# Performance work log

Measured on AMD Instinct MI355X. Metric: run time of the kernel, lower is better.

The kernel has to match this reference:

```python
import jax, jax.numpy as jnp
import numpy as np

N = 50000
E = 400000
IN_DIM = 16
EMB = 32
HID = 128
HEADS = 4
LAYERS = 3
EPS_BN = 1e-5
NEG_SLOPE = 0.2


def setup_inputs() -> dict:
    key = jax.random.key(0)
    ks = jax.random.split(key, 16)
    s = 0.1
    C = HID  # per-head out channels (concat=False)
    inp = {
        "x": jax.random.normal(ks[0], (N, IN_DIM), jnp.float32),
        "edge_index": jax.random.randint(ks[1], (2, E), 0, N, jnp.int64),
        "emb": s * jax.random.normal(ks[2], (N, EMB), jnp.float32),
        "Wf": s * jax.random.normal(ks[3], (EMB, IN_DIM), jnp.float32),
        "bf": jnp.zeros((EMB,), jnp.float32),
        "Wc": s * jax.random.normal(ks[4], (HID, 2 * EMB), jnp.float32),
        "bc": jnp.zeros((HID,), jnp.float32),
        "Wl": s * jax.random.normal(ks[5], (LAYERS, HEADS * C, HID), jnp.float32),
        "a_src": s * jax.random.normal(ks[6], (LAYERS, HEADS, C), jnp.float32),
        "a_dst": s * jax.random.normal(ks[7], (LAYERS, HEADS, C), jnp.float32),
        "bl": jnp.zeros((LAYERS, C), jnp.float32),
        "gamma": jnp.ones((LAYERS, C), jnp.float32),
        "beta": jnp.zeros((LAYERS, C), jnp.float32),
        "Wout": s * jax.random.normal(ks[8], (1, HID), jnp.float32),
        "bout": jnp.zeros((1,), jnp.float32),
    }
    return inp


def _gat_layer(h, src, dst, W, a_s, a_d, b):
    n = h.shape[0]
    C = W.shape[0] // HEADS
    hp = (h @ W.T).reshape(n, HEADS, C)                # (N,H,C)
    al_s = jnp.sum(hp * a_s, axis=-1)                  # (N,H)
    al_d = jnp.sum(hp * a_d, axis=-1)                  # (N,H)
    e = jax.nn.leaky_relu(al_s[src] + al_d[dst], NEG_SLOPE)  # (E,H)
    m = jax.ops.segment_max(e, dst, num_segments=n)    # per-target max
    ex = jnp.exp(e - m[dst])
    denom = jax.ops.segment_sum(ex, dst, num_segments=n) + 1e-16
    alpha = ex / denom[dst]                            # (E,H)
    msg = hp[src] * alpha[..., None]                   # (E,H,C)
    out = jax.ops.segment_sum(msg, dst, num_segments=n)
    return jnp.mean(out, axis=1) + b                   # concat=False: head mean


def _bn(x, g, b):
    mu = jnp.mean(x, axis=0)
    var = jnp.var(x, axis=0)  # biased, as torch BN uses for normalization
    return (x - mu) * jax.lax.rsqrt(var + EPS_BN) * g + b


def reference(x, edge_index, emb, Wf, bf, Wc, bc, Wl, a_src, a_dst, bl, gamma, beta, Wout, bout):
    n = x.shape[0]
    loop = jnp.arange(n, dtype=edge_index.dtype)
    src = jnp.concatenate([edge_index[0], loop])       # add self loops
    dst = jnp.concatenate([edge_index[1], loop])
    feat = x @ Wf.T + bf
    h = jax.nn.relu(jnp.concatenate([emb, feat], axis=1) @ Wc.T + bc)
    prev_h = h
    for i in range(LAYERS):
        h = _gat_layer(h, src, dst, Wl[i], a_src[i], a_dst[i], bl[i])
        h = jax.nn.relu(_bn(h, gamma[i], beta[i]))
        if prev_h.shape == h.shape:
            h = h + prev_h
        prev_h = h
    out = h @ Wout.T + bout
    return jnp.clip(out, -10.0, 10.0)
```

## Files before the change

### kernel.cpp

```cpp
#include <hip/hip_runtime.h>
#include <hip/hip_bf16.h>
#include <math.h>

#define INDIM 16
#define EMBD 32
#define UDIM 64
#define HIDD 128
#define HEADS 4
#define LAYERS 3
#define MPAD 50048

typedef short v8s __attribute__((ext_vector_type(8)));
typedef float v4f __attribute__((ext_vector_type(4)));

__device__ __forceinline__ float lrelu(float x) { return x > 0.f ? x : 0.2f * x; }
__device__ __forceinline__ float bf2f(unsigned int bits16) {
    unsigned int u = bits16 << 16;
    return __builtin_bit_cast(float, u);
}
__device__ __forceinline__ unsigned short f2bf(float f) {
    unsigned int u = __builtin_bit_cast(unsigned int, f);
    unsigned int lsb = (u >> 16) & 1;
    u += 0x7fff + lsb;
    return (unsigned short)(u >> 16);
}

__global__ __launch_bounds__(256) void k_enc(const float* __restrict__ x,
                                             const float* __restrict__ emb,
                                             const float* __restrict__ Wf,
                                             const float* __restrict__ bf,
                                             unsigned short* __restrict__ u, int n) {
    int i = blockIdx.x * 256 + threadIdx.x;
    if (i >= n * EMBD) return;
    int node = i >> 5, j = i & 31;
    const float* xr = x + (size_t)node * INDIM;
    const float* wr = Wf + (size_t)j * INDIM;
    float s = bf[j];
#pragma unroll
    for (int k = 0; k < INDIM; k++) s += xr[k] * wr[k];
    u[(size_t)node * UDIM + EMBD + j] = f2bf(s);
    u[(size_t)node * UDIM + j] = f2bf(emb[(size_t)node * EMBD + j]);
}

__global__ __launch_bounds__(256) void k_prep_v(const float* __restrict__ Wl,
                                                unsigned short* __restrict__ Vb) {
    int i = blockIdx.x * 256 + threadIdx.x;
    if (i >= LAYERS * HIDD * 512) return;
    int l = i >> 16;
    int rem = i & 65535;
    int c = rem >> 9;
    int f = rem & 511;
    int h = f >> 7, k = f & 127;
    Vb[i] = f2bf(Wl[(size_t)l * 512 * HIDD + (size_t)(h * HIDD + c) * HIDD + k]);
}

__global__ __launch_bounds__(256) void k_prep_a(const float* __restrict__ Wl,
                                                const float* __restrict__ a_s,
                                                const float* __restrict__ a_d,
                                                float* __restrict__ ws, float* __restrict__ wd) {
    int i = blockIdx.x * 256 + threadIdx.x;
    if (i >= LAYERS * HEADS * HIDD) return;
    int l = i >> 9, h = (i >> 7) & 3, k = i & 127;
    const float* W = Wl + (size_t)l * 512 * HIDD;
    const float* as = a_s + l * 512 + h * HIDD;
    const float* ad = a_d + l * 512 + h * HIDD;
    float ss = 0.f, sd = 0.f;
    for (int c = 0; c < HIDD; c++) {
        float w = W[(size_t)(h * HIDD + c) * HIDD + k];
        ss += as[c] * w;
        sd += ad[c] * w;
    }
    ws[i] = ss;
    wd[i] = sd;
}

__global__ __launch_bounds__(256) void k_prep_wc(const float* __restrict__ Wc,
                                                 unsigned short* __restrict__ Wcb) {
    int i = blockIdx.x * 256 + threadIdx.x;
    if (i < HIDD * UDIM) Wcb[i] = f2bf(Wc[i]);
}

__global__ __launch_bounds__(256) void k_gemm_enc(const unsigned short* __restrict__ A,
                                                  const unsigned short* __restrict__ B,
                                                  const float* __restrict__ bias,
                                                  float* __restrict__ O,
                                                  unsigned short* __restrict__ Ob, int M) {
    const int K = UDIM;
    int tid = threadIdx.x;
    int lane = tid & 63, wid = tid >> 6;
    int wm = wid >> 1, wn = wid & 1;
    int bm = blockIdx.x * 128;
    int lr = lane & 15, lk = lane >> 4;
    v4f acc[4][4] = {};
    const unsigned short* Abase = A + (size_t)(bm + wm * 64 + lr) * K + lk * 8;
    const unsigned short* Bbase = B + (size_t)(wn * 64 + lr) * K + lk * 8;
#pragma unroll
    for (int kk = 0; kk < K / 32; kk++) {
        v8s a[4], b[4];
#pragma unroll
        for (int f = 0; f < 4; f++) {
            a[f] = *(const v8s*)(Abase + (size_t)(f * 16) * K + kk * 32);
            b[f] = *(const v8s*)(Bbase + (size_t)(f * 16) * K + kk * 32);
        }
#pragma unroll
        for (int i = 0; i < 4; i++)
#pragma unroll
            for (int j = 0; j < 4; j++)
                acc[i][j] = __builtin_amdgcn_mfma_f32_16x16x32_bf16(a[i], b[j], acc[i][j], 0, 0, 0);
    }
#pragma unroll
    for (int i = 0; i < 4; i++) {
#pragma unroll
        for (int r = 0; r < 4; r++) {
            int row = bm + wm * 64 + i * 16 + lk * 4 + r;
            if (row >= M) continue;
#pragma unroll
            for (int j = 0; j < 4; j++) {
                int col = wn * 64 + j * 16 + lr;
                float v = fmaxf(acc[i][j][r] + bias[col], 0.f);
                O[(size_t)row * HIDD + col] = v;
                Ob[(size_t)row * HIDD + col] = f2bf(v);
            }
        }
    }
}

__global__ __launch_bounds__(256) void k_deg(const int* __restrict__ ei, int* __restrict__ deg,
                                             int E, int tot) {
    int e = blockIdx.x * 256 + threadIdx.x;
    if (e >= tot) return;
    int dst = (e < E) ? ei[E + e] : (e - E);
    atomicAdd(&deg[dst], 1);
}

__global__ __launch_bounds__(256) void k_scan1(const int* __restrict__ deg,
                                               int* __restrict__ rowptr,
                                               int* __restrict__ partials, int n) {
    int tid = threadIdx.x;
    int i = blockIdx.x * 256 + tid;
    int v = (i < n) ? deg[i] : 0;
    __shared__ int sm[256];
    sm[tid] = v;
    __syncthreads();
    for (int off = 1; off < 256; off <<= 1) {
        int t = (tid >= off) ? sm[tid - off] : 0;
        __syncthreads();
        sm[tid] += t;
        __syncthreads();
    }
    if (i < n) rowptr[i] = sm[tid] - v;
    if (tid == 255) partials[blockIdx.x] = sm[255];
}

__global__ __launch_bounds__(256) void k_scan2(int* __restrict__ partials, int nb) {
    int tid = threadIdx.x;
    int v = (tid < nb) ? partials[tid] : 0;
    __shared__ int sm[256];
    sm[tid] = v;
    __syncthreads();
    for (int off = 1; off < 256; off <<= 1) {
        int t = (tid >= off) ? sm[tid - off] : 0;
        __syncthreads();
        sm[tid] += t;
        __syncthreads();
    }
    if (tid < nb) partials[tid] = sm[tid] - v;
}

__global__ __launch_bounds__(256) void k_scan3(const int* __restrict__ deg,
                                               const int* __restrict__ partials,
                                               int* __restrict__ rowptr,
                                               int* __restrict__ cursor, int n) {
    int i = blockIdx.x * 256 + threadIdx.x;
    if (i >= n) return;
    int r = rowptr[i] + partials[blockIdx.x];
    rowptr[i] = r;
    cursor[i] = r;
    if (i == n - 1) rowptr[n] = r + deg[i];
}

__global__ __launch_bounds__(256) void k_scatter(const int* __restrict__ ei, int* __restrict__ cursor,
                                                 int* __restrict__ csr_src, int E, int tot) {
    int e = blockIdx.x * 256 + threadIdx.x;
    if (e >= tot) return;
    int src = (e < E) ? ei[e] : (e - E);
    int dst = (e < E) ? ei[E + e] : (e - E);
    int pos = atomicAdd(&cursor[dst], 1);
    csr_src[pos] = src;
}

__global__ __launch_bounds__(256) void k_al0(const float* __restrict__ h,
                                             const float* __restrict__ ws,
                                             const float* __restrict__ wd,
                                             float* __restrict__ al_s, float* __restrict__ al_d,
                                             int n) {
    int wid = threadIdx.x >> 6, lane = threadIdx.x & 63;
    int node = blockIdx.x * 4 + wid;
    if (node >= n) return;
    float2 v = *(const float2*)(h + (size_t)node * HIDD + 2 * lane);
    float s[8];
#pragma unroll
    for (int hh = 0; hh < 4; hh++) {
        float2 w1 = *(const float2*)(ws + hh * HIDD + 2 * lane);
        float2 w2 = *(const float2*)(wd + hh * HIDD + 2 * lane);
        s[hh] = v.x * w1.x + v.y * w1.y;
        s[4 + hh] = v.x * w2.x + v.y * w2.y;
    }
#pragma unroll
    for (int o = 32; o; o >>= 1)
#pragma unroll
        for (int q = 0; q < 8; q++) s[q] += __shfl_xor(s[q], o);
    if (lane == 0) {
        *(float4*)(al_s + (size_t)node * 4) = make_float4(s[0], s[1], s[2], s[3]);
        *(float4*)(al_d + (size_t)node * 4) = make_float4(s[4], s[5], s[6], s[7]);
    }
}

__global__ __launch_bounds__(256) void k_layer(const int* __restrict__ rowptr,
                                               const int* __restrict__ csr_src,
                                               const float* __restrict__ al_s,
                                               const float* __restrict__ al_d,
                                               const unsigned short* __restrict__ hb,
                                               const unsigned short* __restrict__ Vb,
                                               float* __restrict__ agg,
                                               float* __restrict__ bns, int n) {
    __shared__ unsigned short G[16][520];
    __shared__ float s1[128], s2[128];
    int tid = threadIdx.x, lane = tid & 63, wid = tid >> 6;
    if (tid < 128) { s1[tid] = 0.f; s2[tid] = 0.f; }
    int node0 = blockIdx.x * 16;
    const float4* als4 = (const float4*)al_s;
    const unsigned int* h2 = (const unsigned int*)hb;
    unsigned int* Gw = (unsigned int*)G;

    for (int i = 0; i < 4; i++) {
        int lrow = wid * 4 + i;
        int node = node0 + lrow;
        float acc[4][2] = {};
        if (node < n) {
            int start = rowptr[node], end = rowptr[node + 1];
            int deg = end - start;
            float4 ad = ((const float4*)al_d)[node];
            if (deg <= 64) {
                bool act = lane < deg;
                int src_l = act ? csr_src[start + lane] : 0;
                float e0 = -3.0e38f, e1 = -3.0e38f, e2 = -3.0e38f, e3 = -3.0e38f;
                if (act) {
                    float4 as = als4[src_l];
                    e0 = lrelu(as.x + ad.x);
                    e1 = lrelu(as.y + ad.y);
                    e2 = lrelu(as.z + ad.z);
                    e3 = lrelu(as.w + ad.w);
                }
                float m0 = e0, m1 = e1, m2 = e2, m3 = e3;
#pragma unroll
                for (int o = 32; o; o >>= 1) {
                    m0 = fmaxf(m0, __shfl_xor(m0, o));
                    m1 = fmaxf(m1, __shfl_xor(m1, o));
                    m2 = fmaxf(m2, __shfl_xor(m2, o));
                    m3 = fmaxf(m3, __shfl_xor(m3, o));
                }
                float p0 = act ? expf(e0 - m0) : 0.f;
                float p1 = act ? expf(e1 - m1) : 0.f;
                float p2 = act ? expf(e2 - m2) : 0.f;
                float p3 = act ? expf(e3 - m3) : 0.f;
                float t0 = p0, t1 = p1, t2 = p2, t3 = p3;
#pragma unroll
                for (int o = 32; o; o >>= 1) {
                    t0 += __shfl_xor(t0, o);
                    t1 += __shfl_xor(t1, o);
                    t2 += __shfl_xor(t2, o);
                    t3 += __shfl_xor(t3, o);
                }
                float a0 = p0 / (t0 + 1e-16f), a1 = p1 / (t1 + 1e-16f);
                float a2 = p2 / (t2 + 1e-16f), a3 = p3 / (t3 + 1e-16f);
                int jj = 0;
                for (; jj + 2 <= deg; jj += 2) {
                    int sj0 = __shfl(src_l, jj), sj1 = __shfl(src_l, jj + 1);
                    unsigned int u0 = h2[(size_t)sj0 * 64 + lane];
                    unsigned int u1 = h2[(size_t)sj1 * 64 + lane];
                    float b00 = __shfl(a0, jj), b01 = __shfl(a1, jj);
                    float b02 = __shfl(a2, jj), b03 = __shfl(a3, jj);
                    float b10 = __shfl(a0, jj + 1), b11 = __shfl(a1, jj + 1);
                    float b12 = __shfl(a2, jj + 1), b13 = __shfl(a3, jj + 1);
                    float x00 = bf2f(u0 & 0xffff), x01 = bf2f(u0 >> 16);
                    float x10 = bf2f(u1 & 0xffff), x11 = bf2f(u1 >> 16);
                    acc[0][0] += b00 * x00 + b10 * x10; acc[0][1] += b00 * x01 + b10 * x11;
                    acc[1][0] += b01 * x00 + b11 * x10; acc[1][1] += b01 * x01 + b11 * x11;
                    acc[2][0] += b02 * x00 + b12 * x10; acc[2][1] += b02 * x01 + b12 * x11;
                    acc[3][0] += b03 * x00 + b13 * x10; acc[3][1] += b03 * x01 + b13 * x11;
                }
                if (jj < deg) {
                    int sj = __shfl(src_l, jj);
                    unsigned int uu = h2[(size_t)sj * 64 + lane];
                    float b0 = __shfl(a0, jj), b1 = __shfl(a1, jj);
                    float b2 = __shfl(a2, jj), b3 = __shfl(a3, jj);
                    float x0 = bf2f(uu & 0xffff), x1 = bf2f(uu >> 16);
                    acc[0][0] += b0 * x0; acc[0][1] += b0 * x1;
                    acc[1][0] += b1 * x0; acc[1][1] += b1 * x1;
                    acc[2][0] += b2 * x0; acc[2][1] += b2 * x1;
                    acc[3][0] += b3 * x0; acc[3][1] += b3 * x1;
                }
            } else {
                float m0 = -3.0e38f, m1 = -3.0e38f, m2 = -3.0e38f, m3 = -3.0e38f;
                for (int j = start + lane; j < end; j += 64) {
                    float4 as = als4[csr_src[j]];
                    m0 = fmaxf(m0, lrelu(as.x + ad.x));
                    m1 = fmaxf(m1, lrelu(as.y + ad.y));
                    m2 = fmaxf(m2, lrelu(as.z + ad.z));
                    m3 = fmaxf(m3, lrelu(as.w + ad.w));
                }
#pragma unroll
                for (int o = 32; o; o >>= 1) {
                    m0 = fmaxf(m0, __shfl_xor(m0, o));
                    m1 = fmaxf(m1, __shfl_xor(m1, o));
                    m2 = fmaxf(m2, __shfl_xor(m2, o));
                    m3 = fmaxf(m3, __shfl_xor(m3, o));
                }
                float t0 = 0.f, t1 = 0.f, t2 = 0.f, t3 = 0.f;
                for (int j = start + lane; j < end; j += 64) {
                    float4 as = als4[csr_src[j]];
                    t0 += expf(lrelu(as.x + ad.x) - m0);
                    t1 += expf(lrelu(as.y + ad.y) - m1);
                    t2 += expf(lrelu(as.z + ad.z) - m2);
                    t3 += expf(lrelu(as.w + ad.w) - m3);
                }
#pragma unroll
                for (int o = 32; o; o >>= 1) {
                    t0 += __shfl_xor(t0, o);
                    t1 += __shfl_xor(t1, o);
                    t2 += __shfl_xor(t2, o);
                    t3 += __shfl_xor(t3, o);
                }
                float i0 = 1.f / (t0 + 1e-16f), i1 = 1.f / (t1 + 1e-16f);
                float i2 = 1.f / (t2 + 1e-16f), i3 = 1.f / (t3 + 1e-16f);
                for (int base = start; base < end; base += 64) {
                    int cnt = min(64, end - base);
                    bool act = lane < cnt;
                    int src_l = act ? csr_src[base + lane] : 0;
                    float a0 = 0.f, a1 = 0.f, a2 = 0.f, a3 = 0.f;
                    if (act) {
                        float4 as = als4[src_l];
                        a0 = expf(lrelu(as.x + ad.x) - m0) * i0;
                        a1 = expf(lrelu(as.y + ad.y) - m1) * i1;
                        a2 = expf(lrelu(as.z + ad.z) - m2) * i2;
                        a3 = expf(lrelu(as.w + ad.w) - m3) * i3;
                    }
                    for (int jj = 0; jj < cnt; jj++) {
                        int sj = __shfl(src_l, jj);
                        float b0 = __shfl(a0, jj), b1 = __shfl(a1, jj);
                        float b2 = __shfl(a2, jj), b3 = __shfl(a3, jj);
                        unsigned int uu = h2[(size_t)sj * 64 + lane];
                        float x0 = bf2f(uu & 0xffff), x1 = bf2f(uu >> 16);
                        acc[0][0] += b0 * x0; acc[0][1] += b0 * x1;
                        acc[1][0] += b1 * x0; acc[1][1] += b1 * x1;
                        acc[2][0] += b2 * x0; acc[2][1] += b2 * x1;
                        acc[3][0] += b3 * x0; acc[3][1] += b3 * x1;
                    }
                }
            }
        }
#pragma unroll
        for (int hh = 0; hh < 4; hh++) {
            unsigned int p = (unsigned int)f2bf(acc[hh][0]) | ((unsigned int)f2bf(acc[hh][1]) << 16);
            Gw[lrow * 260 + hh * 64 + lane] = p;
        }
    }
    __syncthreads();

    int lr = lane & 15, lk = lane >> 4;
    v4f acc2[2] = {};
#pragma unroll
    for (int kk = 0; kk < 16; kk++) {
        v8s a = *(const v8s*)((const char*)G + lr * 1040 + kk * 64 + lk * 16);
        v8s b0 = *(const v8s*)(Vb + (size_t)(wid * 32 + lr) * 512 + kk * 32 + lk * 8);
        v8s b1 = *(const v8s*)(Vb + (size_t)(wid * 32 + 16 + lr) * 512 + kk * 32 + lk * 8);
        acc2[0] = __builtin_amdgcn_mfma_f32_16x16x32_bf16(a, b0, acc2[0], 0, 0, 0);
        acc2[1] = __builtin_amdgcn_mfma_f32_16x16x32_bf16(a, b1, acc2[1], 0, 0, 0);
    }
#pragma unroll
    for (int j = 0; j < 2; j++) {
        int col = wid * 32 + j * 16 + lr;
        float ls = 0.f, lq = 0.f;
#pragma unroll
        for (int r = 0; r < 4; r++) {
            int node = node0 + lk * 4 + r;
            float v = acc2[j][r];
            if (node < n) {
                agg[(size_t)node * HIDD + col] = v;
                ls += v;
                lq += v * v;
            }
        }
        atomicAdd(&s1[col], ls);
        atomicAdd(&s2[col], lq);
    }
    __syncthreads();
    if (tid < 128) {
        atomicAdd(&bns[tid], s1[tid]);
        atomicAdd(&bns[128 + tid], s2[tid]);
    }
}

template <int MODE>
__global__ __launch_bounds__(256) void k_apply(const float* __restrict__ agg,
                                               const float* __restrict__ bns,
                                               const float* __restrict__ gamma,
                                               const float* __restrict__ beta,
                                               float* __restrict__ h,
                                               unsigned short* __restrict__ hb,
                                               const float* __restrict__ ws,
                                               const float* __restrict__ wd,
                                               float* __restrict__ al_s,
                                               float* __restrict__ al_d,
                                               const float* __restrict__ Wout,
                                               const float* __restrict__ bout,
                                               float* __restrict__ out,
                                               float invn, int n) {
    int wid = threadIdx.x >> 6, lane = threadIdx.x & 63;
    int node = blockIdx.x * 4 + wid;
    if (node >= n) return;
    int c0 = 2 * lane, c1 = 2 * lane + 1;
    float2 ag = *(const float2*)(agg + (size_t)node * HIDD + c0);
    float2 ho = *(const float2*)(h + (size_t)node * HIDD + c0);
    float mu0 = bns[c0] * invn, mu1 = bns[c1] * invn;
    float va0 = bns[128 + c0] * invn - mu0 * mu0;
    float va1 = bns[128 + c1] * invn - mu1 * mu1;
    float sc0 = gamma[c0] * rsqrtf(0.0625f * va0 + 1e-5f);
    float sc1 = gamma[c1] * rsqrtf(0.0625f * va1 + 1e-5f);
    float v0 = fmaxf((ag.x - mu0) * 0.25f * sc0 + beta[c0], 0.f) + ho.x;
    float v1 = fmaxf((ag.y - mu1) * 0.25f * sc1 + beta[c1], 0.f) + ho.y;
    if (MODE == 0) {
        *(float2*)(h + (size_t)node * HIDD + c0) = make_float2(v0, v1);
        ((unsigned int*)hb)[(size_t)node * 64 + lane] =
            (unsigned int)f2bf(v0) | ((unsigned int)f2bf(v1) << 16);
        float s[8];
#pragma unroll
        for (int hh = 0; hh < 4; hh++) {
            float2 w1 = *(const float2*)(ws + hh * HIDD + c0);
            float2 w2 = *(const float2*)(wd + hh * HIDD + c0);
            s[hh] = v0 * w1.x + v1 * w1.y;
            s[4 + hh] = v0 * w2.x + v1 * w2.y;
        }
#pragma unroll
        for (int o = 32; o; o >>= 1)
#pragma unroll
            for (int q = 0; q < 8; q++) s[q] += __shfl_xor(s[q], o);
        if (lane == 0) {
            *(float4*)(al_s + (size_t)node * 4) = make_float4(s[0], s[1], s[2], s[3]);
            *(float4*)(al_d + (size_t)node * 4) = make_float4(s[4], s[5], s[6], s[7]);
        }
    } else {
        float2 w = *(const float2*)(Wout + c0);
        float p = v0 * w.x + v1 * w.y;
#pragma unroll
        for (int o = 32; o; o >>= 1) p += __shfl_xor(p, o);
        if (lane == 0) {
            float v = p + bout[0];
            out[node] = fminf(fmaxf(v, -10.f), 10.f);
        }
    }
}

extern "C" void kernel_launch(void* const* d_in, const int* in_sizes, int n_in,
                              void* d_out, int out_size, void* d_ws, size_t ws_size,
                              hipStream_t stream) {
    const float* x = (const float*)d_in[0];
    const int* ei = (const int*)d_in[1];
    const float* emb = (const float*)d_in[2];
    const float* Wf = (const float*)d_in[3];
    const float* bf = (const float*)d_in[4];
    const float* Wc = (const float*)d_in[5];
    const float* bc = (const float*)d_in[6];
    const float* Wl = (const float*)d_in[7];
    const float* a_src = (const float*)d_in[8];
    const float* a_dst = (const float*)d_in[9];
    const float* gamma = (const float*)d_in[11];
    const float* beta = (const float*)d_in[12];
    const float* Wout = (const float*)d_in[13];
    const float* bout = (const float*)d_in[14];
    float* out = (float*)d_out;

    int n = in_sizes[0] / INDIM;
    int E = in_sizes[1] / 2;
    int tot = E + n;
    int NB = (n + 255) / 256;

    size_t off = 0;
    auto alloc = [&](size_t bytes) {
        void* p = (char*)d_ws + off;
        off = (off + bytes + 255) & ~(size_t)255;
        return p;
    };
    unsigned short* u = (unsigned short*)alloc((size_t)MPAD * UDIM * 2);
    float* h = (float*)alloc((size_t)MPAD * HIDD * 4);
    unsigned short* hb = (unsigned short*)alloc((size_t)MPAD * HIDD * 2);
    float* agg = (float*)alloc((size_t)MPAD * HIDD * 4);
    float* al_s = (float*)alloc((size_t)n * HEADS * 4);
    float* al_d = (float*)alloc((size_t)n * HEADS * 4);
    int* deg = (int*)alloc((size_t)n * 4);
    int* rowptr = (int*)alloc(((size_t)n + 1) * 4);
    int* cursor = (int*)alloc((size_t)n * 4);
    int* csr_src = (int*)alloc((size_t)tot * 4);
    int* partials = (int*)alloc((size_t)NB * 4);
    unsigned short* Vb = (unsigned short*)alloc((size_t)LAYERS * HIDD * 512 * 2);
    unsigned short* Wcb = (unsigned short*)alloc((size_t)HIDD * UDIM * 2);
    float* ws = (float*)alloc((size_t)LAYERS * HEADS * HIDD * 4);
    float* wd = (float*)alloc((size_t)LAYERS * HEADS * HIDD * 4);
    float* bnsums = (float*)alloc(LAYERS * 256 * 4);
    (void)ws_size;

    hipMemsetAsync(deg, 0, (size_t)n * 4, stream);
    hipMemsetAsync(bnsums, 0, LAYERS * 256 * 4, stream);
    if (n < MPAD) {
        hipMemsetAsync(u + (size_t)n * UDIM, 0, (size_t)(MPAD - n) * UDIM * 2, stream);
    }

    k_prep_v<<<(LAYERS * HIDD * 512 + 255) / 256, 256, 0, stream>>>(Wl, Vb);
    k_prep_a<<<(LAYERS * HEADS * HIDD + 255) / 256, 256, 0, stream>>>(Wl, a_src, a_dst, ws, wd);
    k_prep_wc<<<(HIDD * UDIM + 255) / 256, 256, 0, stream>>>(Wc, Wcb);

    k_deg<<<(tot + 255) / 256, 256, 0, stream>>>(ei, deg, E, tot);
    k_scan1<<<NB, 256, 0, stream>>>(deg, rowptr, partials, n);
    k_scan2<<<1, 256, 0, stream>>>(partials, NB);
    k_scan3<<<NB, 256, 0, stream>>>(deg, partials, rowptr, cursor, n);
    k_scatter<<<(tot + 255) / 256, 256, 0, stream>>>(ei, cursor, csr_src, E, tot);

    k_enc<<<(n * EMBD + 255) / 256, 256, 0, stream>>>(x, emb, Wf, bf, u, n);
    k_gemm_enc<<<MPAD / 128, 256, 0, stream>>>(u, Wcb, bc, h, hb, n);
    k_al0<<<(n + 3) / 4, 256, 0, stream>>>(h, ws, wd, al_s, al_d, n);

    float invn = 1.0f / (float)n;
    int NLB = (n + 15) / 16;
    for (int l = 0; l < LAYERS; l++) {
        k_layer<<<NLB, 256, 0, stream>>>(rowptr, csr_src, al_s, al_d, hb,
                                         Vb + (size_t)l * HIDD * 512, agg,
                                         bnsums + l * 256, n);
        if (l < LAYERS - 1)
            k_apply<0><<<(n + 3) / 4, 256, 0, stream>>>(
                agg, bnsums + l * 256, gamma + l * HIDD, beta + l * HIDD, h, hb,
                ws + (size_t)(l + 1) * 512, wd + (size_t)(l + 1) * 512, al_s, al_d,
                nullptr, nullptr, nullptr, invn, n);
        else
            k_apply<1><<<(n + 3) / 4, 256, 0, stream>>>(
                agg, bnsums + l * 256, gamma + l * HIDD, beta + l * HIDD, h, hb,
                nullptr, nullptr, nullptr, nullptr, Wout, bout, out, invn, n);
    }
}
```

Measured before the change: 525.3 us.

## Use one wave per node in 1024-thread GAT layer blocks with swizzled LDS

The layer kernel now launches 16 waves per block, each aggregating one destination node, instead of 4 waves each looping over 4 nodes. Per-node gather latency is spread across more concurrent waves. The LDS tile drops its padding and uses an XOR swizzle to avoid bank conflicts. The MFMA projection now runs on only 8 of 16 waves, each producing 16 output columns. Half the waves sit idle during the GEMM phase, and the larger blocks may change occupancy.

```diff
diff --git a/kernel.cpp b/kernel.cpp
--- a/kernel.cpp
+++ b/kernel.cpp
@@ -216,178 +216,176 @@
     }
 }
 
-__global__ __launch_bounds__(256) void k_layer(const int* __restrict__ rowptr,
-                                               const int* __restrict__ csr_src,
-                                               const float* __restrict__ al_s,
-                                               const float* __restrict__ al_d,
-                                               const unsigned short* __restrict__ hb,
-                                               const unsigned short* __restrict__ Vb,
-                                               float* __restrict__ agg,
-                                               float* __restrict__ bns, int n) {
-    __shared__ unsigned short G[16][520];
+__global__ __launch_bounds__(1024) void k_layer(const int* __restrict__ rowptr,
+                                                const int* __restrict__ csr_src,
+                                                const float* __restrict__ al_s,
+                                                const float* __restrict__ al_d,
+                                                const unsigned short* __restrict__ hb,
+                                                const unsigned short* __restrict__ Vb,
+                                                float* __restrict__ agg,
+                                                float* __restrict__ bns, int n) {
+    __shared__ unsigned int Gw[16 * 256];
     __shared__ float s1[128], s2[128];
-    int tid = threadIdx.x, lane = tid & 63, wid = tid >> 6;
+    int tid = threadIdx.x, lane = tid & 63, w = tid >> 6;
     if (tid < 128) { s1[tid] = 0.f; s2[tid] = 0.f; }
     int node0 = blockIdx.x * 16;
+    int node = node0 + w;
     const float4* als4 = (const float4*)al_s;
     const unsigned int* h2 = (const unsigned int*)hb;
-    unsigned int* Gw = (unsigned int*)G;
-
-    for (int i = 0; i < 4; i++) {
-        int lrow = wid * 4 + i;
-        int node = node0 + lrow;
-        float acc[4][2] = {};
-        if (node < n) {
-            int start = rowptr[node], end = rowptr[node + 1];
-            int deg = end - start;
-            float4 ad = ((const float4*)al_d)[node];
-            if (deg <= 64) {
-                bool act = lane < deg;
-                int src_l = act ? csr_src[start + lane] : 0;
-                float e0 = -3.0e38f, e1 = -3.0e38f, e2 = -3.0e38f, e3 = -3.0e38f;
+    float acc[4][2] = {};
+
+    if (node < n) {
+        int start = rowptr[node], end = rowptr[node + 1];
+        int deg = end - start;
+        float4 ad = ((const float4*)al_d)[node];
+        if (deg <= 64) {
+            bool act = lane < deg;
+            int src_l = act ? csr_src[start + lane] : 0;
+            float e0 = -3.0e38f, e1 = -3.0e38f, e2 = -3.0e38f, e3 = -3.0e38f;
+            if (act) {
+                float4 as = als4[src_l];
+                e0 = lrelu(as.x + ad.x);
+                e1 = lrelu(as.y + ad.y);
+                e2 = lrelu(as.z + ad.z);
+                e3 = lrelu(as.w + ad.w);
+            }
+            float m0 = e0, m1 = e1, m2 = e2, m3 = e3;
+#pragma unroll
+            for (int o = 32; o; o >>= 1) {
+                m0 = fmaxf(m0, __shfl_xor(m0, o));
+                m1 = fmaxf(m1, __shfl_xor(m1, o));
+                m2 = fmaxf(m2, __shfl_xor(m2, o));
+                m3 = fmaxf(m3, __shfl_xor(m3, o));
+            }
+            float p0 = act ? expf(e0 - m0) : 0.f;
+            float p1 = act ? expf(e1 - m1) : 0.f;
+            float p2 = act ? expf(e2 - m2) : 0.f;
+            float p3 = act ? expf(e3 - m3) : 0.f;
+            float t0 = p0, t1 = p1, t2 = p2, t3 = p3;
+#pragma unroll
+            for (int o = 32; o; o >>= 1) {
+                t0 += __shfl_xor(t0, o);
+                t1 += __shfl_xor(t1, o);
+                t2 += __shfl_xor(t2, o);
+                t3 += __shfl_xor(t3, o);
+            }
+            float a0 = p0 / (t0 + 1e-16f), a1 = p1 / (t1 + 1e-16f);
+            float a2 = p2 / (t2 + 1e-16f), a3 = p3 / (t3 + 1e-16f);
+            int jj = 0;
+            for (; jj + 2 <= deg; jj += 2) {
+                int sj0 = __shfl(src_l, jj), sj1 = __shfl(src_l, jj + 1);
+                unsigned int u0 = h2[(size_t)sj0 * 64 + lane];
+                unsigned int u1 = h2[(size_t)sj1 * 64 + lane];
+                float b00 = __shfl(a0, jj), b01 = __shfl(a1, jj);
+                float b02 = __shfl(a2, jj), b03 = __shfl(a3, jj);
+                float b10 = __shfl(a0, jj + 1), b11 = __shfl(a1, jj + 1);
+                float b12 = __shfl(a2, jj + 1), b13 = __shfl(a3, jj + 1);
+                float x00 = bf2f(u0 & 0xffff), x01 = bf2f(u0 >> 16);
+                float x10 = bf2f(u1 & 0xffff), x11 = bf2f(u1 >> 16);
+                acc[0][0] += b00 * x00 + b10 * x10; acc[0][1] += b00 * x01 + b10 * x11;
+                acc[1][0] += b01 * x00 + b11 * x10; acc[1][1] += b01 * x01 + b11 * x11;
+                acc[2][0] += b02 * x00 + b12 * x10; acc[2][1] += b02 * x01 + b12 * x11;
+                acc[3][0] += b03 * x00 + b13 * x10; acc[3][1] += b03 * x01 + b13 * x11;
+            }
+            if (jj < deg) {
+                int sj = __shfl(src_l, jj);
+                unsigned int uu = h2[(size_t)sj * 64 + lane];
+                float b0 = __shfl(a0, jj), b1 = __shfl(a1, jj);
+                float b2 = __shfl(a2, jj), b3 = __shfl(a3, jj);
+                float x0 = bf2f(uu & 0xffff), x1 = bf2f(uu >> 16);
+                acc[0][0] += b0 * x0; acc[0][1] += b0 * x1;
+                acc[1][0] += b1 * x0; acc[1][1] += b1 * x1;
+                acc[2][0] += b2 * x0; acc[2][1] += b2 * x1;
+                acc[3][0] += b3 * x0; acc[3][1] += b3 * x1;
+            }
+        } else {
+            float m0 = -3.0e38f, m1 = -3.0e38f, m2 = -3.0e38f, m3 = -3.0e38f;
+            for (int j = start + lane; j < end; j += 64) {
+                float4 as = als4[csr_src[j]];
+                m0 = fmaxf(m0, lrelu(as.x + ad.x));
+                m1 = fmaxf(m1, lrelu(as.y + ad.y));
+                m2 = fmaxf(m2, lrelu(as.z + ad.z));
+                m3 = fmaxf(m3, lrelu(as.w + ad.w));
+            }
+#pragma unroll
+            for (int o = 32; o; o >>= 1) {
+                m0 = fmaxf(m0, __shfl_xor(m0, o));
+                m1 = fmaxf(m1, __shfl_xor(m1, o));
+                m2 = fmaxf(m2, __shfl_xor(m2, o));
+                m3 = fmaxf(m3, __shfl_xor(m3, o));
+            }
+            float t0 = 0.f, t1 = 0.f, t2 = 0.f, t3 = 0.f;
+            for (int j = start + lane; j < end; j += 64) {
+                float4 as = als4[csr_src[j]];
+                t0 += expf(lrelu(as.x + ad.x) - m0);
+                t1 += expf(lrelu(as.y + ad.y) - m1);
+                t2 += expf(lrelu(as.z + ad.z) - m2);
+                t3 += expf(lrelu(as.w + ad.w) - m3);
+            }
+#pragma unroll
+            for (int o = 32; o; o >>= 1) {
+                t0 += __shfl_xor(t0, o);
+                t1 += __shfl_xor(t1, o);
+                t2 += __shfl_xor(t2, o);
+                t3 += __shfl_xor(t3, o);
+            }
+            float i0 = 1.f / (t0 + 1e-16f), i1 = 1.f / (t1 + 1e-16f);
+            float i2 = 1.f / (t2 + 1e-16f), i3 = 1.f / (t3 + 1e-16f);
+            for (int base = start; base < end; base += 64) {
+                int cnt = min(64, end - base);
+                bool act = lane < cnt;
+                int src_l = act ? csr_src[base + lane] : 0;
+                float a0 = 0.f, a1 = 0.f, a2 = 0.f, a3 = 0.f;
                 if (act) {
                     float4 as = als4[src_l];
-                    e0 = lrelu(as.x + ad.x);
-                    e1 = lrelu(as.y + ad.y);
-                    e2 = lrelu(as.z + ad.z);
-                    e3 = lrelu(as.w + ad.w);
+                    a0 = expf(lrelu(as.x + ad.x) - m0) * i0;
+                    a1 = expf(lrelu(as.y + ad.y) - m1) * i1;
+                    a2 = expf(lrelu(as.z + ad.z) - m2) * i2;
+                    a3 = expf(lrelu(as.w + ad.w) - m3) * i3;
                 }
-                float m0 = e0, m1 = e1, m2 = e2, m3 = e3;
-#pragma unroll
-                for (int o = 32; o; o >>= 1) {
-                    m0 = fmaxf(m0, __shfl_xor(m0, o));
-                    m1 = fmaxf(m1, __shfl_xor(m1, o));
-                    m2 = fmaxf(m2, __shfl_xor(m2, o));
-                    m3 = fmaxf(m3, __shfl_xor(m3, o));
-                }
-                float p0 = act ? expf(e0 - m0) : 0.f;
-                float p1 = act ? expf(e1 - m1) : 0.f;
-                float p2 = act ? expf(e2 - m2) : 0.f;
-                float p3 = act ? expf(e3 - m3) : 0.f;
-                float t0 = p0, t1 = p1, t2 = p2, t3 = p3;
-#pragma unroll
-                for (int o = 32; o; o >>= 1) {
-                    t0 += __shfl_xor(t0, o);
-                    t1 += __shfl_xor(t1, o);
-                    t2 += __shfl_xor(t2, o);
-                    t3 += __shfl_xor(t3, o);
-                }
-                float a0 = p0 / (t0 + 1e-16f), a1 = p1 / (t1 + 1e-16f);
-                float a2 = p2 / (t2 + 1e-16f), a3 = p3 / (t3 + 1e-16f);
-                int jj = 0;
-                for (; jj + 2 <= deg; jj += 2) {
-                    int sj0 = __shfl(src_l, jj), sj1 = __shfl(src_l, jj + 1);
-                    unsigned int u0 = h2[(size_t)sj0 * 64 + lane];
-                    unsigned int u1 = h2[(size_t)sj1 * 64 + lane];
-                    float b00 = __shfl(a0, jj), b01 = __shfl(a1, jj);
-                    float b02 = __shfl(a2, jj), b03 = __shfl(a3, jj);
-                    float b10 = __shfl(a0, jj + 1), b11 = __shfl(a1, jj + 1);
-                    float b12 = __shfl(a2, jj + 1), b13 = __shfl(a3, jj + 1);
-                    float x00 = bf2f(u0 & 0xffff), x01 = bf2f(u0 >> 16);
-                    float x10 = bf2f(u1 & 0xffff), x11 = bf2f(u1 >> 16);
-                    acc[0][0] += b00 * x00 + b10 * x10; acc[0][1] += b00 * x01 + b10 * x11;
-                    acc[1][0] += b01 * x00 + b11 * x10; acc[1][1] += b01 * x01 + b11 * x11;
-                    acc[2][0] += b02 * x00 + b12 * x10; acc[2][1] += b02 * x01 + b12 * x11;
-                    acc[3][0] += b03 * x00 + b13 * x10; acc[3][1] += b03 * x01 + b13 * x11;
-                }
-                if (jj < deg) {
+                for (int jj = 0; jj < cnt; jj++) {
                     int sj = __shfl(src_l, jj);
-                    unsigned int uu = h2[(size_t)sj * 64 + lane];
                     float b0 = __shfl(a0, jj), b1 = __shfl(a1, jj);
                     float b2 = __shfl(a2, jj), b3 = __shfl(a3, jj);
+                    unsigned int uu = h2[(size_t)sj * 64 + lane];
                     float x0 = bf2f(uu & 0xffff), x1 = bf2f(uu >> 16);
                     acc[0][0] += b0 * x0; acc[0][1] += b0 * x1;
                     acc[1][0] += b1 * x0; acc[1][1] += b1 * x1;
                     acc[2][0] += b2 * x0; acc[2][1] += b2 * x1;
                     acc[3][0] += b3 * x0; acc[3][1] += b3 * x1;
                 }
-            } else {
-                float m0 = -3.0e38f, m1 = -3.0e38f, m2 = -3.0e38f, m3 = -3.0e38f;
-                for (int j = start + lane; j < end; j += 64) {
-                    float4 as = als4[csr_src[j]];
-                    m0 = fmaxf(m0, lrelu(as.x + ad.x));
-                    m1 = fmaxf(m1, lrelu(as.y + ad.y));
-                    m2 = fmaxf(m2, lrelu(as.z + ad.z));
-                    m3 = fmaxf(m3, lrelu(as.w + ad.w));
-                }
-#pragma unroll
-                for (int o = 32; o; o >>= 1) {
-                    m0 = fmaxf(m0, __shfl_xor(m0, o));
-                    m1 = fmaxf(m1, __shfl_xor(m1, o));
-                    m2 = fmaxf(m2, __shfl_xor(m2, o));
-                    m3 = fmaxf(m3, __shfl_xor(m3, o));
-                }
-                float t0 = 0.f, t1 = 0.f, t2 = 0.f, t3 = 0.f;
-                for (int j = start + lane; j < end; j += 64) {
-                    float4 as = als4[csr_src[j]];
-                    t0 += expf(lrelu(as.x + ad.x) - m0);
-                    t1 += expf(lrelu(as.y + ad.y) - m1);
-                    t2 += expf(lrelu(as.z + ad.z) - m2);
-                    t3 += expf(lrelu(as.w + ad.w) - m3);
-                }
-#pragma unroll
-                for (int o = 32; o; o >>= 1) {
-                    t0 += __shfl_xor(t0, o);
-                    t1 += __shfl_xor(t1, o);
-                    t2 += __shfl_xor(t2, o);
-                    t3 += __shfl_xor(t3, o);
-                }
-                float i0 = 1.f / (t0 + 1e-16f), i1 = 1.f / (t1 + 1e-16f);
-                float i2 = 1.f / (t2 + 1e-16f), i3 = 1.f / (t3 + 1e-16f);
-                for (int base = start; base < end; base += 64) {
-                    int cnt = min(64, end - base);
-                    bool act = lane < cnt;
-                    int src_l = act ? csr_src[base + lane] : 0;
-                    float a0 = 0.f, a1 = 0.f, a2 = 0.f, a3 = 0.f;
-                    if (act) {
-                        float4 as = als4[src_l];
-                        a0 = expf(lrelu(as.x + ad.x) - m0) * i0;
-                        a1 = expf(lrelu(as.y + ad.y) - m1) * i1;
-                        a2 = expf(lrelu(as.z + ad.z) - m2) * i2;
-                        a3 = expf(lrelu(as.w + ad.w) - m3) * i3;
-                    }
-                    for (int jj = 0; jj < cnt; jj++) {
-                        int sj = __shfl(src_l, jj);
-                        float b0 = __shfl(a0, jj), b1 = __shfl(a1, jj);
-                        float b2 = __shfl(a2, jj), b3 = __shfl(a3, jj);
-                        unsigned int uu = h2[(size_t)sj * 64 + lane];
-                        float x0 = bf2f(uu & 0xffff), x1 = bf2f(uu >> 16);
-                        acc[0][0] += b0 * x0; acc[0][1] += b0 * x1;
-                        acc[1][0] += b1 * x0; acc[1][1] += b1 * x1;
-                        acc[2][0] += b2 * x0; acc[2][1] += b2 * x1;
-                        acc[3][0] += b3 * x0; acc[3][1] += b3 * x1;
-                    }
-                }
-            }
-        }
+            }
+        }
+    }
+    {
+        int sw = (w & 7) << 2;
 #pragma unroll
         for (int hh = 0; hh < 4; hh++) {
             unsigned int p = (unsigned int)f2bf(acc[hh][0]) | ((unsigned int)f2bf(acc[hh][1]) << 16);
-            Gw[lrow * 260 + hh * 64 + lane] = p;
+            Gw[w * 256 + ((hh * 64 + lane) ^ sw)] = p;
         }
     }
     __syncthreads();
 
-    int lr = lane & 15, lk = lane >> 4;
-    v4f acc2[2] = {};
-#pragma unroll
-    for (int kk = 0; kk < 16; kk++) {
-        v8s a = *(const v8s*)((const char*)G + lr * 1040 + kk * 64 + lk * 16);
-        v8s b0 = *(const v8s*)(Vb + (size_t)(wid * 32 + lr) * 512 + kk * 32 + lk * 8);
-        v8s b1 = *(const v8s*)(Vb + (size_t)(wid * 32 + 16 + lr) * 512 + kk * 32 + lk * 8);
-        acc2[0] = __builtin_amdgcn_mfma_f32_16x16x32_bf16(a, b0, acc2[0], 0, 0, 0);
-        acc2[1] = __builtin_amdgcn_mfma_f32_16x16x32_bf16(a, b1, acc2[1], 0, 0, 0);
-    }
-#pragma unroll
-    for (int j = 0; j < 2; j++) {
-        int col = wid * 32 + j * 16 + lr;
+    if (w < 8) {
+        int lr = lane & 15, lk = lane >> 4;
+        int swr = (lr & 7) << 2;
+        v4f a2 = {};
+        const unsigned short* Bb = Vb + (size_t)(w * 16 + lr) * 512 + lk * 8;
+#pragma unroll
+        for (int kk = 0; kk < 16; kk++) {
+            v8s a = *(const v8s*)(&Gw[lr * 256 + ((kk * 16 + lk * 4) ^ swr)]);
+            v8s b = *(const v8s*)(Bb + kk * 32);
+            a2 = __builtin_amdgcn_mfma_f32_16x16x32_bf16(a, b, a2, 0, 0, 0);
+        }
+        int col = w * 16 + lr;
         float ls = 0.f, lq = 0.f;
 #pragma unroll
         for (int r = 0; r < 4; r++) {
-            int node = node0 + lk * 4 + r;
-            float v = acc2[j][r];
-            if (node < n) {
-                agg[(size_t)node * HIDD + col] = v;
+            int nd = node0 + lk * 4 + r;
+            float v = a2[r];
+            if (nd < n) {
+                agg[(size_t)nd * HIDD + col] = v;
                 ls += v;
                 lq += v * v;
             }
@@ -533,9 +531,9 @@
     float invn = 1.0f / (float)n;
     int NLB = (n + 15) / 16;
     for (int l = 0; l < LAYERS; l++) {
-        k_layer<<<NLB, 256, 0, stream>>>(rowptr, csr_src, al_s, al_d, hb,
-                                         Vb + (size_t)l * HIDD * 512, agg,
-                                         bnsums + l * 256, n);
+        k_layer<<<NLB, 1024, 0, stream>>>(rowptr, csr_src, al_s, al_d, hb,
+                                          Vb + (size_t)l * HIDD * 512, agg,
+                                          bnsums + l * 256, n);
         if (l < LAYERS - 1)
             k_apply<0><<<(n + 3) / 4, 256, 0, stream>>>(
                 agg, bnsums + l * 256, gamma + l * HIDD, beta + l * HIDD, h, hb,
```

Measured after the change: 512.0 us. 2.5% less time.
